# Kernel optimization log

Hardware: AMD Instinct MI355X
Metric: run time of the kernel (lower is better)

## Reference

```python
import jax, jax.numpy as jnp
import numpy as np

B, P = 65536, 22  # sets, max players per freeze frame
IN, HID, OUT = 6, 64, 128


def setup_inputs() -> dict:
    key = jax.random.key(0)
    k0, k1, k2, k3, k4, k5 = jax.random.split(key, 6)
    pitch = jnp.array([120.0, 80.0], dtype=jnp.float32)
    player_locs = jax.random.uniform(k0, (B, P, 2), dtype=jnp.float32) * pitch
    actor_locs = jax.random.uniform(k1, (B, 2), dtype=jnp.float32) * pitch
    # teammate / keeper flags in {0,1}
    flags = jax.random.randint(k2, (B, P, 2), 0, 2).astype(jnp.float32)
    # validity mask: 0 -> player skipped (simulates ragged / missing entries)
    mask = jax.random.randint(k3, (B, P), 0, 2).astype(jnp.int32)
    W1 = jax.random.normal(k4, (IN, HID), dtype=jnp.float32) / np.sqrt(IN)
    b1 = jnp.zeros((HID,), dtype=jnp.float32)
    W2 = jax.random.normal(k5, (HID, OUT), dtype=jnp.float32) / np.sqrt(HID)
    b2 = jnp.zeros((OUT,), dtype=jnp.float32)
    return {"player_locs": player_locs, "actor_locs": actor_locs, "flags": flags,
            "mask": mask, "W1": W1, "b1": b1, "W2": W2, "b2": b2}


def reference(player_locs, actor_locs, flags, mask, W1, b1, W2, b2):
    # per-player features relative to the actor: [dx, dy, dist, angle, teammate, keeper]
    dxy = player_locs - actor_locs[:, None, :]                 # [B,P,2]
    dist = jnp.sqrt(jnp.sum(dxy * dxy, axis=-1, keepdims=True))  # [B,P,1]
    angle = jnp.arctan2(dxy[..., 1:2], dxy[..., 0:1])            # [B,P,1]
    feats = jnp.concatenate([dxy, dist, angle, flags], axis=-1)  # [B,P,6]
    # PlayerMLP: Linear -> ReLU -> Linear
    h = jax.nn.relu(jnp.einsum('bpi,ih->bph', feats, W1) + b1)   # [B,P,64]
    emb = jnp.einsum('bph,ho->bpo', h, W2) + b2                  # [B,P,128]
    # masked mean over valid players; empty sets yield zeros (sum is 0)
    m = mask.astype(emb.dtype)[..., None]                        # [B,P,1]
    cnt = jnp.sum(m, axis=1)                                     # [B,1]
    pooled = jnp.sum(emb * m, axis=1) / jnp.maximum(cnt, 1.0)    # [B,128]
    return pooled
```

## Files before the change

kernel.cpp:

```cpp
#include <hip/hip_runtime.h>
#include <math.h>

#define PMAX 22
#define HID 64
#define OUTD 128
#define SETS_PER_WAVE 8
#define WAVES_PER_BLOCK 4

typedef __attribute__((ext_vector_type(4))) float float4v;
typedef _Float16 fh2 __attribute__((ext_vector_type(2)));
typedef _Float16 half8 __attribute__((ext_vector_type(8)));

__device__ __forceinline__ int rl_i(int v, int l) {
    return __builtin_amdgcn_readlane(v, l);
}
__device__ __forceinline__ int pk2(float x, float y) {
    auto v = __builtin_amdgcn_cvt_pkrtz(x, y);
    union { decltype(v) h; int i; } c;
    c.h = v;
    return c.i;
}
__device__ __forceinline__ unsigned short f16b(float x) {
    return (unsigned short)(pk2(x, x) & 0xFFFF);
}
__device__ __forceinline__ float fdot2i(int a, int b, float c) {
    union { int i; fh2 h; } ua, ub;
    ua.i = a;
    ub.i = b;
#if defined(__has_builtin) && __has_builtin(__builtin_amdgcn_fdot2)
    return __builtin_amdgcn_fdot2(ua.h, ub.h, c, false);
#else
    return fmaf((float)ua.h.x, (float)ub.h.x, fmaf((float)ua.h.y, (float)ub.h.y, c));
#endif
}
__device__ __forceinline__ void wave_lds_sync() {
    asm volatile("s_waitcnt lgkmcnt(0)" ::: "memory");
    __builtin_amdgcn_wave_barrier();
}
__device__ __forceinline__ float fast_atan2(float y, float x) {
    float ax = fabsf(x), ay = fabsf(y);
    float mn = fminf(ax, ay), mx = fmaxf(ax, ay);
    float a = mn * __builtin_amdgcn_rcpf(fmaxf(mx, 1e-30f));
    float s = a * a;
    float r = a * fmaf(s, fmaf(s, fmaf(s, -0.0851330f, 0.1801410f), -0.3302995f), 0.9998660f);
    if (ay > ax) r = 1.57079637f - r;
    if (x < 0.0f) r = 3.14159274f - r;
    return copysignf(r, y);
}

__global__ __launch_bounds__(256) void set_encoder_kernel(
    const float* __restrict__ player_locs,
    const float* __restrict__ actor_locs,
    const float* __restrict__ flags,
    const int*   __restrict__ mask,
    const float* __restrict__ W1,
    const float* __restrict__ b1,
    const float* __restrict__ W2,
    const float* __restrict__ b2,
    float* __restrict__ out)
{
    __shared__ __align__(16) unsigned w2f[16 * 256];
    __shared__ __align__(16) unsigned short hb[WAVES_PER_BLOCK][SETS_PER_WAVE][72];

    const int tid  = threadIdx.x;
    const int lane = tid & 63;
    const int wave = tid >> 6;

    const int wave_id = blockIdx.x * WAVES_PER_BLOCK + wave;
    const int set0    = wave_id * SETS_PER_WAVE;

    {
        const int pr = tid >> 3;
        const int nt = tid & 7;
        const float* rA = W2 + (size_t)(2 * pr) * OUTD + 16 * nt;
        const float* rB = rA + OUTD;
        float ra[16], rb[16];
#pragma unroll
        for (int i = 0; i < 4; ++i) {
            *(float4*)&ra[4 * i] = ((const float4*)rA)[i];
            *(float4*)&rb[4 * i] = ((const float4*)rB)[i];
        }
        const int kt = pr >> 4;
        const int kk = (2 * pr) & 31;
        const int Q  = kk >> 3;
        const int j2 = (kk >> 1) & 3;
        const int base = ((kt * 8 + nt) * 4 + Q) * 64 + j2;
#pragma unroll
        for (int c = 0; c < 16; ++c)
            w2f[base + 4 * c] = pk2(ra[c], rb[c]);
    }

    const int w01 = pk2(W1[0 * HID + lane], W1[1 * HID + lane]);
    const int w23 = pk2(W1[2 * HID + lane], W1[3 * HID + lane]);
    const int w45 = pk2(W1[4 * HID + lane], W1[5 * HID + lane]);
    const float b1l = b1[lane];

    __syncthreads();

    int fh[4][3];
    unsigned long long wbm[4];
    {
        const int lidx = lane < 2 * PMAX ? lane : 2 * PMAX - 1;
        const size_t r0 = (size_t)set0 * PMAX + lidx;
        const float2* plb = (const float2*)player_locs + r0;
        const float2* flb = (const float2*)flags + r0;
        const int*    mkb = mask + r0;
        const float2* acb = (const float2*)actor_locs + set0 + (lidx >= PMAX ? 1 : 0);
#pragma unroll
        for (int g = 0; g < 4; ++g) {
            float2 pl = plb[g * 2 * PMAX];
            float2 fl = flb[g * 2 * PMAX];
            int    m  = mkb[g * 2 * PMAX];
            float2 ac = acb[2 * g];
            float dx = pl.x - ac.x;
            float dy = pl.y - ac.y;
            float dist = __builtin_amdgcn_sqrtf(fmaf(dx, dx, dy * dy));
            float ang  = fast_atan2(dy, dx);
            fh[g][0] = pk2(dx, dy);
            fh[g][1] = pk2(dist, ang);
            fh[g][2] = pk2(fl.x, fl.y);
            unsigned long long bl = __ballot((lane < 2 * PMAX) && (m != 0));
            const unsigned lo = __builtin_amdgcn_readfirstlane((unsigned)bl);
            const unsigned hi = __builtin_amdgcn_readfirstlane((unsigned)(bl >> 32));
            wbm[g] = ((unsigned long long)hi << 32) | lo;
        }
    }

    unsigned nonempty = 0;
#pragma unroll
    for (int s = 0; s < SETS_PER_WAVE; ++s) {
        const int g    = s >> 1;
        const int base = (s & 1) * PMAX;
        const unsigned bits = (unsigned)(wbm[g] >> base) & 0x3FFFFFu;
        const int cnt = __builtin_popcount(bits);
        if (bits) nonempty |= (1u << s);
        float acc = 0.0f;
#pragma unroll
        for (int p = 0; p < PMAX; ++p) {
            if (bits & (1u << p)) {
                float t = fdot2i(rl_i(fh[g][0], base + p), w01, b1l);
                t = fdot2i(rl_i(fh[g][1], base + p), w23, t);
                t = fdot2i(rl_i(fh[g][2], base + p), w45, t);
                acc += fmaxf(t, 0.0f);
            }
        }
        const float hbar = acc * (1.0f / fmaxf((float)cnt, 1.0f));
        hb[wave][s][lane] = f16b(hbar);
    }
    wave_lds_sync();

    const int Q   = lane >> 4;
    const int c15 = lane & 15;
    const int sA  = lane & 7;
    half8 afrag[2];
#pragma unroll
    for (int kt = 0; kt < 2; ++kt) {
        union { uint4 u4; half8 h8; } cv;
        cv.u4 = *(const uint4*)&hb[wave][sA][kt * 32 + Q * 8];
        afrag[kt] = cv.h8;
    }

    float4v acc[8];
#pragma unroll
    for (int nt = 0; nt < 8; ++nt) {
        union { uint4 u4; half8 h8; } f0, f1;
        f0.u4 = *(const uint4*)&w2f[(0 * 8 + nt) * 256 + 4 * lane];
        f1.u4 = *(const uint4*)&w2f[(1 * 8 + nt) * 256 + 4 * lane];
        float4v z = {0.0f, 0.0f, 0.0f, 0.0f};
        acc[nt] = __builtin_amdgcn_mfma_f32_16x16x32_f16(afrag[0], f0.h8, z, 0, 0, 0);
        acc[nt] = __builtin_amdgcn_mfma_f32_16x16x32_f16(afrag[1], f1.h8, acc[nt], 0, 0, 0);
    }

    if (Q < 2) {
        float fs[4];
#pragma unroll
        for (int r = 0; r < 4; ++r) fs[r] = (float)((nonempty >> (4 * Q + r)) & 1u);

        const float* b2b = b2 + c15;
        float b2v[8];
#pragma unroll
        for (int nt = 0; nt < 8; ++nt) b2v[nt] = b2b[16 * nt];

        float* obase = out + (size_t)(set0 + 4 * Q) * OUTD + c15;
#pragma unroll
        for (int nt = 0; nt < 8; ++nt) {
#pragma unroll
            for (int r = 0; r < 4; ++r)
                obase[r * OUTD + nt * 16] = fmaf(fs[r], b2v[nt], acc[nt][r]);
        }
    }
}

extern "C" void kernel_launch(void* const* d_in, const int* in_sizes, int n_in,
                              void* d_out, int out_size, void* d_ws, size_t ws_size,
                              hipStream_t stream) {
    const float* player_locs = (const float*)d_in[0];
    const float* actor_locs  = (const float*)d_in[1];
    const float* flags       = (const float*)d_in[2];
    const int*   mask        = (const int*)d_in[3];
    const float* W1          = (const float*)d_in[4];
    const float* b1          = (const float*)d_in[5];
    const float* W2          = (const float*)d_in[6];
    const float* b2          = (const float*)d_in[7];
    float*       out         = (float*)d_out;

    const int B = in_sizes[0] / (PMAX * 2);
    const int sets_per_block = WAVES_PER_BLOCK * SETS_PER_WAVE;
    const int grid = (B + sets_per_block - 1) / sets_per_block;

    hipLaunchKernelGGL(set_encoder_kernel, dim3(grid), dim3(256), 0, stream,
                       player_locs, actor_locs, flags, mask, W1, b1, W2, b2, out);
}
```

Measured before the change: 110.6 us.

## Process two chunks per block with register prefetch and split output stores

Each block now handles two chunks of sets, so the W2 LDS fragment setup is shared across more work, and the next chunk's raw inputs are prefetched into registers while the current chunk is computed. The input load is issued before the W2 packing and barrier to overlap global latency. The output store is split so all 64 lanes write (two half-column ranges) instead of only half the lanes, and the divide is replaced with rcp. Risks are higher register pressure under launch_bounds(256,4) and half as many blocks in the grid.

```diff
diff --git a/kernel.cpp b/kernel.cpp
--- a/kernel.cpp
+++ b/kernel.cpp
@@ -6,6 +6,7 @@
 #define OUTD 128
 #define SETS_PER_WAVE 8
 #define WAVES_PER_BLOCK 4
+#define CHUNKS 2
 
 typedef __attribute__((ext_vector_type(4))) float float4v;
 typedef _Float16 fh2 __attribute__((ext_vector_type(2)));
@@ -48,7 +49,26 @@
     return copysignf(r, y);
 }
 
-__global__ __launch_bounds__(256) void set_encoder_kernel(
+__device__ __forceinline__ void prefetch_raw(
+    const float* __restrict__ player_locs, const float* __restrict__ flags,
+    const int* __restrict__ mask, const float* __restrict__ actor_locs,
+    int set0, int lidx, float2 pl[4], float2 fl[4], float2 ac[4], int mk[4])
+{
+    const size_t r0 = (size_t)set0 * PMAX + lidx;
+    const float2* plb = (const float2*)player_locs + r0;
+    const float2* flb = (const float2*)flags + r0;
+    const int*    mkb = mask + r0;
+    const float2* acb = (const float2*)actor_locs + set0 + (lidx >= PMAX ? 1 : 0);
+#pragma unroll
+    for (int g = 0; g < 4; ++g) {
+        pl[g] = plb[g * 2 * PMAX];
+        fl[g] = flb[g * 2 * PMAX];
+        mk[g] = mkb[g * 2 * PMAX];
+        ac[g] = acb[2 * g];
+    }
+}
+
+__global__ __launch_bounds__(256, 4) void set_encoder_kernel(
     const float* __restrict__ player_locs,
     const float* __restrict__ actor_locs,
     const float* __restrict__ flags,
@@ -66,127 +86,133 @@
     const int lane = tid & 63;
     const int wave = tid >> 6;
 
-    const int wave_id = blockIdx.x * WAVES_PER_BLOCK + wave;
-    const int set0    = wave_id * SETS_PER_WAVE;
-
+    const int bset = blockIdx.x * (CHUNKS * WAVES_PER_BLOCK * SETS_PER_WAVE);
+
+    const int pr  = tid >> 3;
+    const int nt8 = tid & 7;
+    float ra[16], rb[16];
     {
-        const int pr = tid >> 3;
-        const int nt = tid & 7;
-        const float* rA = W2 + (size_t)(2 * pr) * OUTD + 16 * nt;
+        const float* rA = W2 + (size_t)(2 * pr) * OUTD + 16 * nt8;
         const float* rB = rA + OUTD;
-        float ra[16], rb[16];
 #pragma unroll
         for (int i = 0; i < 4; ++i) {
             *(float4*)&ra[4 * i] = ((const float4*)rA)[i];
             *(float4*)&rb[4 * i] = ((const float4*)rB)[i];
         }
-        const int kt = pr >> 4;
-        const int kk = (2 * pr) & 31;
-        const int Q  = kk >> 3;
-        const int j2 = (kk >> 1) & 3;
-        const int base = ((kt * 8 + nt) * 4 + Q) * 64 + j2;
-#pragma unroll
-        for (int c = 0; c < 16; ++c)
-            w2f[base + 4 * c] = pk2(ra[c], rb[c]);
-    }
+    }
+
+    const int lidx = lane < 2 * PMAX ? lane : 2 * PMAX - 1;
+    float2 pl[4], fl[4], ac2[4];
+    int    mk[4];
+    prefetch_raw(player_locs, flags, mask, actor_locs,
+                 bset + wave * SETS_PER_WAVE, lidx, pl, fl, ac2, mk);
 
     const int w01 = pk2(W1[0 * HID + lane], W1[1 * HID + lane]);
     const int w23 = pk2(W1[2 * HID + lane], W1[3 * HID + lane]);
     const int w45 = pk2(W1[4 * HID + lane], W1[5 * HID + lane]);
     const float b1l = b1[lane];
 
+    const int c15 = lane & 15;
+    const int Q   = lane >> 4;
+    const int sA  = lane & 7;
+    const int sq  = Q & 1;
+    const int nh  = lane >> 5;
+    float b2v[4];
+#pragma unroll
+    for (int k = 0; k < 4; ++k) b2v[k] = b2[64 * nh + 16 * k + c15];
+
+    {
+        const int kt = pr >> 4;
+        const int kk = (2 * pr) & 31;
+        const int Qs = kk >> 3;
+        const int j2 = (kk >> 1) & 3;
+        const int sbase = ((kt * 8 + nt8) * 4 + Qs) * 64 + j2;
+#pragma unroll
+        for (int c = 0; c < 16; ++c)
+            w2f[sbase + 4 * c] = pk2(ra[c], rb[c]);
+    }
+
     __syncthreads();
 
-    int fh[4][3];
-    unsigned long long wbm[4];
-    {
-        const int lidx = lane < 2 * PMAX ? lane : 2 * PMAX - 1;
-        const size_t r0 = (size_t)set0 * PMAX + lidx;
-        const float2* plb = (const float2*)player_locs + r0;
-        const float2* flb = (const float2*)flags + r0;
-        const int*    mkb = mask + r0;
-        const float2* acb = (const float2*)actor_locs + set0 + (lidx >= PMAX ? 1 : 0);
+#pragma unroll
+    for (int c = 0; c < CHUNKS; ++c) {
+        const int set0 = bset + c * (WAVES_PER_BLOCK * SETS_PER_WAVE) + wave * SETS_PER_WAVE;
+
+        int fh[4][3];
+        unsigned long long wbm[4];
 #pragma unroll
         for (int g = 0; g < 4; ++g) {
-            float2 pl = plb[g * 2 * PMAX];
-            float2 fl = flb[g * 2 * PMAX];
-            int    m  = mkb[g * 2 * PMAX];
-            float2 ac = acb[2 * g];
-            float dx = pl.x - ac.x;
-            float dy = pl.y - ac.y;
+            float dx = pl[g].x - ac2[g].x;
+            float dy = pl[g].y - ac2[g].y;
             float dist = __builtin_amdgcn_sqrtf(fmaf(dx, dx, dy * dy));
             float ang  = fast_atan2(dy, dx);
             fh[g][0] = pk2(dx, dy);
             fh[g][1] = pk2(dist, ang);
-            fh[g][2] = pk2(fl.x, fl.y);
-            unsigned long long bl = __ballot((lane < 2 * PMAX) && (m != 0));
+            fh[g][2] = pk2(fl[g].x, fl[g].y);
+            unsigned long long bl = __ballot((lane < 2 * PMAX) && (mk[g] != 0));
             const unsigned lo = __builtin_amdgcn_readfirstlane((unsigned)bl);
             const unsigned hi = __builtin_amdgcn_readfirstlane((unsigned)(bl >> 32));
             wbm[g] = ((unsigned long long)hi << 32) | lo;
         }
-    }
-
-    unsigned nonempty = 0;
-#pragma unroll
-    for (int s = 0; s < SETS_PER_WAVE; ++s) {
-        const int g    = s >> 1;
-        const int base = (s & 1) * PMAX;
-        const unsigned bits = (unsigned)(wbm[g] >> base) & 0x3FFFFFu;
-        const int cnt = __builtin_popcount(bits);
-        if (bits) nonempty |= (1u << s);
-        float acc = 0.0f;
-#pragma unroll
-        for (int p = 0; p < PMAX; ++p) {
-            if (bits & (1u << p)) {
-                float t = fdot2i(rl_i(fh[g][0], base + p), w01, b1l);
-                t = fdot2i(rl_i(fh[g][1], base + p), w23, t);
-                t = fdot2i(rl_i(fh[g][2], base + p), w45, t);
-                acc += fmaxf(t, 0.0f);
+
+        if (c + 1 < CHUNKS)
+            prefetch_raw(player_locs, flags, mask, actor_locs,
+                         bset + (c + 1) * (WAVES_PER_BLOCK * SETS_PER_WAVE) + wave * SETS_PER_WAVE,
+                         lidx, pl, fl, ac2, mk);
+
+        unsigned nonempty = 0;
+#pragma unroll
+        for (int s = 0; s < SETS_PER_WAVE; ++s) {
+            const int g    = s >> 1;
+            const int base = (s & 1) * PMAX;
+            const unsigned bits = (unsigned)(wbm[g] >> base) & 0x3FFFFFu;
+            const int cnt = __builtin_popcount(bits);
+            if (bits) nonempty |= (1u << s);
+            float accv = 0.0f;
+#pragma unroll
+            for (int p = 0; p < PMAX; ++p) {
+                if (bits & (1u << p)) {
+                    float t = fdot2i(rl_i(fh[g][0], base + p), w01, b1l);
+                    t = fdot2i(rl_i(fh[g][1], base + p), w23, t);
+                    t = fdot2i(rl_i(fh[g][2], base + p), w45, t);
+                    accv += fmaxf(t, 0.0f);
+                }
             }
-        }
-        const float hbar = acc * (1.0f / fmaxf((float)cnt, 1.0f));
-        hb[wave][s][lane] = f16b(hbar);
-    }
-    wave_lds_sync();
-
-    const int Q   = lane >> 4;
-    const int c15 = lane & 15;
-    const int sA  = lane & 7;
-    half8 afrag[2];
-#pragma unroll
-    for (int kt = 0; kt < 2; ++kt) {
-        union { uint4 u4; half8 h8; } cv;
-        cv.u4 = *(const uint4*)&hb[wave][sA][kt * 32 + Q * 8];
-        afrag[kt] = cv.h8;
-    }
-
-    float4v acc[8];
-#pragma unroll
-    for (int nt = 0; nt < 8; ++nt) {
-        union { uint4 u4; half8 h8; } f0, f1;
-        f0.u4 = *(const uint4*)&w2f[(0 * 8 + nt) * 256 + 4 * lane];
-        f1.u4 = *(const uint4*)&w2f[(1 * 8 + nt) * 256 + 4 * lane];
-        float4v z = {0.0f, 0.0f, 0.0f, 0.0f};
-        acc[nt] = __builtin_amdgcn_mfma_f32_16x16x32_f16(afrag[0], f0.h8, z, 0, 0, 0);
-        acc[nt] = __builtin_amdgcn_mfma_f32_16x16x32_f16(afrag[1], f1.h8, acc[nt], 0, 0, 0);
-    }
-
-    if (Q < 2) {
+            const float hbar = accv * __builtin_amdgcn_rcpf(fmaxf((float)cnt, 1.0f));
+            hb[wave][s][lane] = f16b(hbar);
+        }
+        wave_lds_sync();
+
+        half8 afrag[2];
+#pragma unroll
+        for (int kt = 0; kt < 2; ++kt) {
+            union { uint4 u4; half8 h8; } cv;
+            cv.u4 = *(const uint4*)&hb[wave][sA][kt * 32 + Q * 8];
+            afrag[kt] = cv.h8;
+        }
+
+        float4v acc[8];
+#pragma unroll
+        for (int nt = 0; nt < 8; ++nt) {
+            union { uint4 u4; half8 h8; } f0, f1;
+            f0.u4 = *(const uint4*)&w2f[(0 * 8 + nt) * 256 + 4 * lane];
+            f1.u4 = *(const uint4*)&w2f[(1 * 8 + nt) * 256 + 4 * lane];
+            float4v z = {0.0f, 0.0f, 0.0f, 0.0f};
+            acc[nt] = __builtin_amdgcn_mfma_f32_16x16x32_f16(afrag[0], f0.h8, z, 0, 0, 0);
+            acc[nt] = __builtin_amdgcn_mfma_f32_16x16x32_f16(afrag[1], f1.h8, acc[nt], 0, 0, 0);
+        }
+
         float fs[4];
 #pragma unroll
-        for (int r = 0; r < 4; ++r) fs[r] = (float)((nonempty >> (4 * Q + r)) & 1u);
-
-        const float* b2b = b2 + c15;
-        float b2v[8];
-#pragma unroll
-        for (int nt = 0; nt < 8; ++nt) b2v[nt] = b2b[16 * nt];
-
-        float* obase = out + (size_t)(set0 + 4 * Q) * OUTD + c15;
-#pragma unroll
-        for (int nt = 0; nt < 8; ++nt) {
+        for (int r = 0; r < 4; ++r) fs[r] = (float)((nonempty >> (4 * sq + r)) & 1u);
+
+        float* obase = out + (size_t)(set0 + 4 * sq) * OUTD + 64 * nh + c15;
+#pragma unroll
+        for (int k = 0; k < 4; ++k) {
+            float4v av = nh ? acc[4 + k] : acc[k];
 #pragma unroll
             for (int r = 0; r < 4; ++r)
-                obase[r * OUTD + nt * 16] = fmaf(fs[r], b2v[nt], acc[nt][r]);
+                obase[r * OUTD + 16 * k] = fmaf(fs[r], b2v[k], av[r]);
         }
     }
 }
@@ -205,7 +231,7 @@
     float*       out         = (float*)d_out;
 
     const int B = in_sizes[0] / (PMAX * 2);
-    const int sets_per_block = WAVES_PER_BLOCK * SETS_PER_WAVE;
+    const int sets_per_block = CHUNKS * WAVES_PER_BLOCK * SETS_PER_WAVE;
     const int grid = (B + sets_per_block - 1) / sets_per_block;
 
     hipLaunchKernelGGL(set_encoder_kernel, dim3(grid), dim3(256), 0, stream,
```

After: 120.0 us. 8.5% more time.
